# Kernel tuning notes

Hardware: AMD Instinct MI355X
Metric: run time of the kernel (lower is better)

Reference implementation:

```python
import jax, jax.numpy as jnp
import numpy as np

N, D_IN, H, OUT, L = 6144, 512, 512, 256, 3
EPS = 1e-5


def setup_inputs() -> dict:
    key = jax.random.key(0)
    ks = jax.random.split(key, 32)
    inp = {}
    inp["X"] = jax.random.normal(ks[0], (N, D_IN), dtype=jnp.float32)
    inp["adj"] = jax.random.randint(ks[1], (N, N), 0, 2).astype(jnp.float32)
    inp["adj_glo"] = jax.random.randint(ks[2], (N, N), 0, 2).astype(jnp.float32)
    s = 1.0 / np.sqrt(H)
    # projection + its BN
    inp["Wp"] = jax.random.normal(ks[3], (H, D_IN), dtype=jnp.float32) / np.sqrt(D_IN)
    inp["bp"] = jnp.zeros((H,), jnp.float32)
    inp["gp"] = jnp.ones((H,), jnp.float32)
    inp["betap"] = jnp.zeros((H,), jnp.float32)
    # per-layer params; layers 0,1 output H, layer 2 outputs OUT
    outs = [H, H, OUT]
    for i in range(L):
        o = outs[i]
        k = jax.random.split(ks[4 + i], 6)
        inp[f"Wq{i}"] = jax.random.normal(k[0], (H, H), jnp.float32) * s
        inp[f"Wk{i}"] = jax.random.normal(k[1], (H, H), jnp.float32) * s
        inp[f"Wv{i}"] = jax.random.normal(k[2], (H, H), jnp.float32) * s
        inp[f"Wo{i}"] = jax.random.normal(k[3], (o, H), jnp.float32) * s
        inp[f"bo{i}"] = jnp.zeros((o,), jnp.float32)
        inp[f"g{i}"] = jnp.ones((o,), jnp.float32)
        inp[f"beta{i}"] = jnp.zeros((o,), jnp.float32)
    return inp


def _normalize_adj(a):
    # symmetric GCN normalization D^{-1/2} A D^{-1/2}
    d = a.sum(axis=1)
    dis = jnp.where(d > 0, jax.lax.rsqrt(jnp.maximum(d, 1e-12)), 0.0)
    return a * dis[:, None] * dis[None, :]


def _bn(x, g, b):
    # BatchNorm1d, training mode: batch stats, biased variance
    m = x.mean(axis=0)
    v = x.var(axis=0)
    return g * (x - m) * jax.lax.rsqrt(v + EPS) + b


def _attn(h, adj, Wq, Wk, Wv, Wo, bo):
    Q = h @ Wq.T
    K = h @ Wk.T
    V = h @ Wv.T
    scores = (Q @ K.T) / np.sqrt(H)            # [N, N]
    scores = jnp.where(adj == 0, -jnp.inf, scores)
    attn = jax.nn.softmax(scores, axis=-1)
    return (attn @ V) @ Wo.T + bo


def reference(X, adj, adj_glo, Wp, bp, gp, betap,
              Wq0, Wk0, Wv0, Wo0, bo0, g0, beta0,
              Wq1, Wk1, Wv1, Wo1, bo1, g1, beta1,
              Wq2, Wk2, Wv2, Wo2, bo2, g2, beta2):
    # embedding: normalized global adjacency aggregation + projection + BN
    h = _normalize_adj(adj_glo) @ X
    h = h @ Wp.T + bp
    h = _bn(h, gp, betap)
    embed_features = h
    layers = [
        (Wq0, Wk0, Wv0, Wo0, bo0, g0, beta0),
        (Wq1, Wk1, Wv1, Wo1, bo1, g1, beta1),
        (Wq2, Wk2, Wv2, Wo2, bo2, g2, beta2),
    ]
    for i, (Wq, Wk, Wv, Wo, bo, g, b) in enumerate(layers):
        h_s = h
        h = _attn(h, adj, Wq, Wk, Wv, Wo, bo)
        h = jax.nn.relu(_bn(h, g, b))
        if i != L - 1:
            h = h + h_s
    return h, embed_features
```

## Files before the change

kernel.cpp:

```cpp
#include <hip/hip_runtime.h>
#include <cstdint>

#define NROW 6144
#define HDIM 512
#define DOUT 256
#define NEG_INF (-__builtin_inff())

typedef _Float16 half8 __attribute__((ext_vector_type(8)));
typedef _Float16 half4v __attribute__((ext_vector_type(4)));
typedef float f32x4 __attribute__((ext_vector_type(4)));

#define BARRIER() asm volatile("s_barrier" ::: "memory")
#define LGKM0()   asm volatile("s_waitcnt lgkmcnt(0)" ::: "memory")
#define VMCNT4()  asm volatile("s_waitcnt vmcnt(4)" ::: "memory")
#define VMCNT0()  asm volatile("s_waitcnt vmcnt(0)" ::: "memory")

__device__ __forceinline__ void gld_lds16(void* lds, const void* g) {
  __builtin_amdgcn_global_load_lds(
      (const __attribute__((address_space(1))) void*)g,
      (__attribute__((address_space(3))) void*)lds, 16, 0, 0);
}

__global__ __launch_bounds__(512, 2)
void gemm256(const _Float16* __restrict__ A, int lda,
             const _Float16* __restrict__ B, int ldb,
             _Float16* __restrict__ C, int ldc, int Kc, long MN)
{
  __shared__ _Float16 As[2][256][64];
  __shared__ _Float16 Bs[2][256][64];
  const int tid = threadIdx.x;
  const int wave = tid >> 6, lane = tid & 63;
  const int wr = wave >> 2, wc = wave & 3;

  const int gx = gridDim.x, gy = gridDim.y;
  const int nwg = gx * gy * gridDim.z;
  int lin = (blockIdx.z * gy + blockIdx.y) * gx + blockIdx.x;
  int swz = (nwg % 8 == 0) ? ((lin % 8) * (nwg >> 3) + (lin >> 3)) : lin;
  const int bx = swz % gx, by = (swz / gx) % gy, bz = swz / (gx * gy);
  const int row0 = bx * 256, col0 = by * 256;
  const _Float16* Ab = A + (size_t)row0 * lda + (size_t)bz * Kc;
  const _Float16* Bb = B + (size_t)col0 * ldb + (size_t)bz * Kc;
  const int nt = Kc >> 6;

  const int srow = lane >> 3;
  const int sgr  = (lane & 7) ^ srow;

  auto stageA = [&](int buf, int h, int t) {
    const _Float16* src = Ab + (size_t)(h * 128 + wave * 8 + srow) * lda + t * 64 + sgr * 8;
    gld_lds16(&As[buf][h * 128 + wave * 8][0], src);
    gld_lds16(&As[buf][h * 128 + 64 + wave * 8][0], src + (size_t)64 * lda);
  };
  auto stageB = [&](int buf, int h, int t) {
    const _Float16* src = Bb + (size_t)(h * 128 + wave * 8 + srow) * ldb + t * 64 + sgr * 8;
    gld_lds16(&Bs[buf][h * 128 + wave * 8][0], src);
    gld_lds16(&Bs[buf][h * 128 + 64 + wave * 8][0], src + (size_t)64 * ldb);
  };

  const int fr = lane & 15, sq = lane >> 4, fx = fr & 7;
  half8 af[4][2], bLo[2][2], bHi[2][2];
  f32x4 acc[8][4];
  const f32x4 vzero = {0.f, 0.f, 0.f, 0.f};
  #pragma unroll
  for (int f = 0; f < 8; ++f)
    #pragma unroll
    for (int j = 0; j < 4; ++j)
      acc[f][j] = vzero;

  auto dsA = [&](int buf, int mh) {
    #pragma unroll
    for (int i = 0; i < 4; ++i)
      #pragma unroll
      for (int ks = 0; ks < 2; ++ks)
        af[i][ks] = *(const half8*)&As[buf][wr * 128 + mh * 64 + i * 16 + fr]
                                          [((ks * 4 + sq) ^ fx) * 8];
  };
  auto dsBlo = [&](int buf) {
    #pragma unroll
    for (int jj = 0; jj < 2; ++jj)
      #pragma unroll
      for (int ks = 0; ks < 2; ++ks)
        bLo[jj][ks] = *(const half8*)&Bs[buf][wc * 64 + jj * 16 + fr]
                                            [((ks * 4 + sq) ^ fx) * 8];
  };
  auto dsBhi = [&](int buf) {
    #pragma unroll
    for (int jj = 0; jj < 2; ++jj)
      #pragma unroll
      for (int ks = 0; ks < 2; ++ks)
        bHi[jj][ks] = *(const half8*)&Bs[buf][wc * 64 + 32 + jj * 16 + fr]
                                            [((ks * 4 + sq) ^ fx) * 8];
  };
  auto mQlo = [&](int fb) {
    __builtin_amdgcn_s_setprio(1);
    #pragma unroll
    for (int i = 0; i < 4; ++i)
      #pragma unroll
      for (int jj = 0; jj < 2; ++jj)
        #pragma unroll
        for (int ks = 0; ks < 2; ++ks)
          acc[fb + i][jj] = __builtin_amdgcn_mfma_f32_16x16x32_f16(
              af[i][ks], bLo[jj][ks], acc[fb + i][jj], 0, 0, 0);
    __builtin_amdgcn_s_setprio(0);
  };
  auto mQhi = [&](int fb) {
    __builtin_amdgcn_s_setprio(1);
    #pragma unroll
    for (int i = 0; i < 4; ++i)
      #pragma unroll
      for (int jj = 0; jj < 2; ++jj)
        #pragma unroll
        for (int ks = 0; ks < 2; ++ks)
          acc[fb + i][2 + jj] = __builtin_amdgcn_mfma_f32_16x16x32_f16(
              af[i][ks], bHi[jj][ks], acc[fb + i][2 + jj], 0, 0, 0);
    __builtin_amdgcn_s_setprio(0);
  };

  stageA(0, 0, 0); stageA(0, 1, 0); stageB(0, 0, 0); stageB(0, 1, 0);
  stageB(1, 0, 1); stageB(1, 1, 1);
  VMCNT4();
  BARRIER();

  for (int T = 0; T < nt; T += 2) {
    const bool pipe = (T + 2 < nt);
    dsA(0, 0); dsBlo(0);
    stageA(1, 0, T + 1);
    BARRIER(); LGKM0(); mQlo(0); BARRIER();
    dsBhi(0);
    stageA(1, 1, T + 1);
    BARRIER(); LGKM0(); mQhi(0); BARRIER();
    dsA(0, 1);
    if (pipe) stageB(0, 0, T + 2);
    BARRIER(); LGKM0(); mQhi(4); BARRIER();
    if (pipe) { stageB(0, 1, T + 2); VMCNT4(); } else { VMCNT0(); }
    BARRIER(); mQlo(4); BARRIER();
    dsA(1, 0); dsBlo(1);
    if (pipe) stageA(0, 0, T + 2);
    BARRIER(); LGKM0(); mQlo(0); BARRIER();
    dsBhi(1);
    if (pipe) stageA(0, 1, T + 2);
    BARRIER(); LGKM0(); mQhi(0); BARRIER();
    dsA(1, 1);
    if (pipe) stageB(1, 0, T + 3);
    BARRIER(); LGKM0(); mQhi(4); BARRIER();
    if (pipe) { stageB(1, 1, T + 3); VMCNT4(); } else { VMCNT0(); }
    BARRIER(); mQlo(4); BARRIER();
  }

  _Float16* dst = C + (size_t)bz * MN;
  #pragma unroll
  for (int f = 0; f < 8; ++f)
    #pragma unroll
    for (int j = 0; j < 4; ++j)
      #pragma unroll
      for (int r = 0; r < 4; ++r) {
        int row = row0 + wr * 128 + f * 16 + sq * 4 + r;
        int col = col0 + wc * 64 + j * 16 + fr;
        dst[(size_t)row * ldc + col] = (_Float16)acc[f][j][r];
      }
}

__global__ __launch_bounds__(256)
void gemm_f16(const _Float16* __restrict__ A, int lda,
              const _Float16* __restrict__ B, int ldb,
              float* __restrict__ Cf, _Float16* __restrict__ Ch, int ldc,
              int Kc, _Float16* __restrict__ Pk, long MN)
{
  __shared__ _Float16 As[128][32];
  __shared__ _Float16 Bs[128][32];
  const int tid = threadIdx.x;
  const int wave = tid >> 6, lane = tid & 63;
  const int wr = wave >> 1, wc = wave & 1;
  const int row0 = blockIdx.x * 128, col0 = blockIdx.y * 128;
  const int kbase = blockIdx.z * Kc;

  const int sr = lane >> 2;
  const int sk = ((lane & 3) ^ ((lane >> 3) & 3)) * 8;

  f32x4 acc[4][4];
  const f32x4 vzero = {0.f, 0.f, 0.f, 0.f};
  #pragma unroll
  for (int i = 0; i < 4; ++i)
    #pragma unroll
    for (int j = 0; j < 4; ++j)
      acc[i][j] = vzero;

  const int fr = lane & 15;
  const int fk = (((lane >> 4) ^ ((fr >> 1) & 3))) * 8;

  for (int k0 = kbase; k0 < kbase + Kc; k0 += 32) {
    #pragma unroll
    for (int c = 0; c < 2; ++c) {
      int rbase = c * 64 + wave * 16;
      gld_lds16(&As[rbase][0], A + (size_t)(row0 + rbase + sr) * lda + k0 + sk);
      gld_lds16(&Bs[rbase][0], B + (size_t)(col0 + rbase + sr) * ldb + k0 + sk);
    }
    __syncthreads();
    half8 af[4], bf[4];
    #pragma unroll
    for (int i = 0; i < 4; ++i)
      af[i] = *(const half8*)&As[wr * 64 + i * 16 + fr][fk];
    #pragma unroll
    for (int j = 0; j < 4; ++j)
      bf[j] = *(const half8*)&Bs[wc * 64 + j * 16 + fr][fk];
    #pragma unroll
    for (int i = 0; i < 4; ++i)
      #pragma unroll
      for (int j = 0; j < 4; ++j)
        acc[i][j] = __builtin_amdgcn_mfma_f32_16x16x32_f16(af[i], bf[j], acc[i][j], 0, 0, 0);
    __syncthreads();
  }

  const int lr = (lane >> 4) * 4;
  const int lc = lane & 15;
  if (Pk) {
    _Float16* dst = Pk + (size_t)blockIdx.z * MN;
    #pragma unroll
    for (int i = 0; i < 4; ++i)
      #pragma unroll
      for (int j = 0; j < 4; ++j)
        #pragma unroll
        for (int r = 0; r < 4; ++r) {
          int row = row0 + wr * 64 + i * 16 + lr + r;
          int col = col0 + wc * 64 + j * 16 + lc;
          dst[(size_t)row * ldc + col] = (_Float16)acc[i][j][r];
        }
    return;
  }
  #pragma unroll
  for (int i = 0; i < 4; ++i)
    #pragma unroll
    for (int j = 0; j < 4; ++j)
      #pragma unroll
      for (int r = 0; r < 4; ++r) {
        int row = row0 + wr * 64 + i * 16 + lr + r;
        int col = col0 + wc * 64 + j * 16 + lc;
        float v = acc[i][j][r];
        if (Cf) Cf[(size_t)row * ldc + col] = v;
        if (Ch) Ch[(size_t)row * ldc + col] = (_Float16)v;
      }
}

__global__ __launch_bounds__(256)
void reduce_splitk(const _Float16* __restrict__ Pk, long MN, int S, int cshift,
                   const float* __restrict__ rowscale,
                   float* __restrict__ Yf, _Float16* __restrict__ Yh)
{
  long n4 = MN >> 2;
  for (long i = (long)blockIdx.x * 256 + threadIdx.x; i < n4; i += (long)gridDim.x * 256) {
    float s0 = 0, s1 = 0, s2 = 0, s3 = 0;
    for (int z = 0; z < S; ++z) {
      half4v p = ((const half4v*)(Pk + (size_t)z * MN))[i];
      s0 += (float)p[0]; s1 += (float)p[1]; s2 += (float)p[2]; s3 += (float)p[3];
    }
    if (rowscale) {
      float sc = rowscale[(i * 4) >> cshift];
      s0 *= sc; s1 *= sc; s2 *= sc; s3 *= sc;
    }
    if (Yf) {
      float4 o; o.x = s0; o.y = s1; o.z = s2; o.w = s3;
      ((float4*)Yf)[i] = o;
    }
    if (Yh) {
      half4v o;
      o[0] = (_Float16)s0; o[1] = (_Float16)s1; o[2] = (_Float16)s2; o[3] = (_Float16)s3;
      ((half4v*)Yh)[i] = o;
    }
  }
}

__global__ __launch_bounds__(256)
void degree_convert(const float* __restrict__ A, _Float16* __restrict__ Ah,
                    float* __restrict__ dis)
{
  const int row = blockIdx.x;
  const float* a = A + (size_t)row * NROW;
  _Float16* o = Ah + (size_t)row * NROW;
  float s = 0.f;
  #pragma unroll
  for (int it = 0; it < 6; ++it) {
    int j = it * 1024 + threadIdx.x * 4;
    float4 v = *(const float4*)&a[j];
    s += v.x + v.y + v.z + v.w;
    half4v h;
    h[0] = (_Float16)v.x; h[1] = (_Float16)v.y; h[2] = (_Float16)v.z; h[3] = (_Float16)v.w;
    *(half4v*)&o[j] = h;
  }
  #pragma unroll
  for (int off = 32; off; off >>= 1) s += __shfl_xor(s, off);
  __shared__ float red[4];
  if ((threadIdx.x & 63) == 0) red[threadIdx.x >> 6] = s;
  __syncthreads();
  if (threadIdx.x == 0) {
    float d = red[0] + red[1] + red[2] + red[3];
    dis[row] = (d > 0.f) ? rsqrtf(fmaxf(d, 1e-12f)) : 0.f;
  }
}

__global__ __launch_bounds__(192)
void build_mask(const float* __restrict__ adj, uint32_t* __restrict__ bits)
{
  const int row = blockIdx.x;
  const int w = threadIdx.x;
  const float* a = adj + (size_t)row * NROW + w * 32;
  uint32_t m = 0;
  #pragma unroll
  for (int q = 0; q < 8; ++q) {
    float4 x = *(const float4*)&a[q * 4];
    m |= (x.x != 0.f ? 1u : 0u) << (q * 4 + 0);
    m |= (x.y != 0.f ? 1u : 0u) << (q * 4 + 1);
    m |= (x.z != 0.f ? 1u : 0u) << (q * 4 + 2);
    m |= (x.w != 0.f ? 1u : 0u) << (q * 4 + 3);
  }
  bits[(size_t)row * 192 + w] = m;
}

struct WConv {
  const float* src[13];
  _Float16* dst[13];
  int n4[13];
  float scale[13];
};
__global__ __launch_bounds__(256)
void convert_weights(WConv w)
{
  const int seg = blockIdx.x >> 4;
  const int bi = blockIdx.x & 15;
  const float* x = w.src[seg];
  _Float16* y = w.dst[seg];
  const float sc = w.scale[seg];
  const int n4 = w.n4[seg];
  for (int i = bi * 256 + threadIdx.x; i < n4; i += 16 * 256) {
    float4 v = ((const float4*)x)[i];
    half4v o;
    o[0] = (_Float16)(v.x * sc); o[1] = (_Float16)(v.y * sc);
    o[2] = (_Float16)(v.z * sc); o[3] = (_Float16)(v.w * sc);
    ((half4v*)y)[i] = o;
  }
}

__global__ __launch_bounds__(256)
void transpose_scale_f16(const float* __restrict__ src, const float* __restrict__ rowscale,
                         _Float16* __restrict__ dst, int R, int C)
{
  __shared__ _Float16 tile[64][72];
  const int c0 = blockIdx.x * 64, r0 = blockIdx.y * 64;
  const int tx4 = (threadIdx.x & 15) * 4, ty = threadIdx.x >> 4;
  #pragma unroll
  for (int p = 0; p < 4; ++p) {
    int r = p * 16 + ty;
    float4 v = *(const float4*)&src[(size_t)(r0 + r) * C + c0 + tx4];
    float sc = rowscale ? rowscale[r0 + r] : 1.0f;
    tile[tx4 + 0][r] = (_Float16)(v.x * sc);
    tile[tx4 + 1][r] = (_Float16)(v.y * sc);
    tile[tx4 + 2][r] = (_Float16)(v.z * sc);
    tile[tx4 + 3][r] = (_Float16)(v.w * sc);
  }
  __syncthreads();
  #pragma unroll
  for (int p = 0; p < 4; ++p) {
    int c = p * 16 + ty;
    half4v o;
    o[0] = tile[c][tx4 + 0];
    o[1] = tile[c][tx4 + 1];
    o[2] = tile[c][tx4 + 2];
    o[3] = tile[c][tx4 + 3];
    *(half4v*)&dst[(size_t)(c0 + c) * R + r0 + tx4] = o;
  }
}

__global__ __launch_bounds__(256)
void transpose_f16(const _Float16* __restrict__ src, int ld,
                   _Float16* __restrict__ dst, int R, int C)
{
  __shared__ _Float16 tile[64][72];
  const int c0 = blockIdx.x * 64, r0 = blockIdx.y * 64;
  const int tx4 = (threadIdx.x & 15) * 4, ty = threadIdx.x >> 4;
  #pragma unroll
  for (int p = 0; p < 4; ++p) {
    int r = p * 16 + ty;
    half4v v = *(const half4v*)&src[(size_t)(r0 + r) * ld + c0 + tx4];
    tile[tx4 + 0][r] = v[0];
    tile[tx4 + 1][r] = v[1];
    tile[tx4 + 2][r] = v[2];
    tile[tx4 + 3][r] = v[3];
  }
  __syncthreads();
  #pragma unroll
  for (int p = 0; p < 4; ++p) {
    int c = p * 16 + ty;
    half4v o;
    o[0] = tile[c][tx4 + 0];
    o[1] = tile[c][tx4 + 1];
    o[2] = tile[c][tx4 + 2];
    o[3] = tile[c][tx4 + 3];
    *(half4v*)&dst[(size_t)(c0 + c) * R + r0 + tx4] = o;
  }
}

__global__ __launch_bounds__(256)
void softmax_mask16(_Float16* __restrict__ Sf, const uint32_t* __restrict__ bits,
                    float* __restrict__ linv)
{
  const int row = blockIdx.x;
  _Float16* s = Sf + (size_t)row * NROW;
  const uint32_t* b = bits + (size_t)row * 192;
  const int tid = threadIdx.x;
  float v[24];
  float m = NEG_INF;
  #pragma unroll
  for (int it = 0; it < 3; ++it) {
    int j = it * 2048 + tid * 8;
    half8 sv = *(const half8*)&s[j];
    uint32_t w = (b[j >> 5] >> (j & 31)) & 0xffu;
    #pragma unroll
    for (int e = 0; e < 8; ++e) {
      float x = ((w >> e) & 1u) ? (float)sv[e] : NEG_INF;
      v[it * 8 + e] = x;
      m = fmaxf(m, x);
    }
  }
  #pragma unroll
  for (int off = 32; off; off >>= 1) m = fmaxf(m, __shfl_xor(m, off));
  __shared__ float red[4];
  const int lane = tid & 63, wave = tid >> 6;
  if (lane == 0) red[wave] = m;
  __syncthreads();
  m = fmaxf(fmaxf(red[0], red[1]), fmaxf(red[2], red[3]));
  __syncthreads();
  float l = 0.f;
  #pragma unroll
  for (int k = 0; k < 24; ++k) {
    float e = (v[k] == NEG_INF) ? 0.f : __expf(v[k] - m);
    v[k] = e; l += e;
  }
  #pragma unroll
  for (int off = 32; off; off >>= 1) l += __shfl_xor(l, off);
  if (lane == 0) red[wave] = l;
  __syncthreads();
  l = red[0] + red[1] + red[2] + red[3];
  if (tid == 0) linv[row] = (l > 0.f) ? (1.f / l) : 0.f;
  #pragma unroll
  for (int it = 0; it < 3; ++it) {
    int j = it * 2048 + tid * 8;
    half8 o;
    #pragma unroll
    for (int e = 0; e < 8; ++e) o[e] = (_Float16)v[it * 8 + e];
    *(half8*)&s[j] = o;
  }
}

__global__ __launch_bounds__(256)
void bn_partial(const _Float16* __restrict__ X, int C,
                float* __restrict__ psum, float* __restrict__ psq)
{
  const int b = blockIdx.x;
  const int t = threadIdx.x;
  const int tpc = C >> 3;
  const int ng = 256 / tpc;
  const int g = t / tpc, c8 = (t % tpc) * 8;
  const int rpg = 64 / ng;
  const _Float16* x = X + (size_t)b * 64 * C;
  float s[8], q[8];
  #pragma unroll
  for (int e = 0; e < 8; ++e) { s[e] = 0.f; q[e] = 0.f; }
  for (int r = g * rpg; r < (g + 1) * rpg; ++r) {
    half8 v = *(const half8*)&x[(size_t)r * C + c8];
    #pragma unroll
    for (int e = 0; e < 8; ++e) {
      float f = (float)v[e];
      s[e] += f; q[e] += f * f;
    }
  }
  __shared__ float ls[256][8], lq[256][8];
  #pragma unroll
  for (int e = 0; e < 8; ++e) { ls[t][e] = s[e]; lq[t][e] = q[e]; }
  __syncthreads();
  for (int u = t; u < C; u += 256) {
    float ss = 0, qq = 0;
    for (int gg = 0; gg < ng; ++gg) {
      ss += ls[gg * tpc + (u >> 3)][u & 7];
      qq += lq[gg * tpc + (u >> 3)][u & 7];
    }
    psum[b * C + u] = ss; psq[b * C + u] = qq;
  }
}

__global__ void bn_finalize(const float* __restrict__ psum, const float* __restrict__ psq,
                            int C, const float* __restrict__ g, const float* __restrict__ beta,
                            float* __restrict__ scale, float* __restrict__ shift)
{
  int c = threadIdx.x + blockIdx.x * blockDim.x;
  if (c >= C) return;
  float s = 0, q = 0;
  for (int b = 0; b < 96; ++b) { s += psum[b * C + c]; q += psq[b * C + c]; }
  const float invN = 1.0f / 6144.0f;
  float mean = s * invN;
  float var = q * invN - mean * mean;
  float rstd = rsqrtf(fmaxf(var, 0.f) + 1e-5f);
  float sc = g[c] * rstd;
  scale[c] = sc;
  shift[c] = beta[c] - mean * sc;
}

__global__ __launch_bounds__(256)
void bn_apply(const _Float16* __restrict__ X, const float* __restrict__ scale,
              const float* __restrict__ shift, const _Float16* __restrict__ residual,
              float* __restrict__ Yf, _Float16* __restrict__ Yh,
              int Cmask, long total, int do_relu)
{
  for (long i = (long)blockIdx.x * 256 + threadIdx.x; i < total; i += (long)gridDim.x * 256) {
    int c = (int)(i & Cmask);
    float v = (float)X[i] * scale[c] + shift[c];
    if (do_relu) v = fmaxf(v, 0.f);
    if (residual) v += (float)residual[i];
    if (Yf) Yf[i] = v;
    if (Yh) Yh[i] = (_Float16)v;
  }
}

extern "C" void kernel_launch(void* const* d_in, const int* in_sizes, int n_in,
                              void* d_out, int out_size, void* d_ws, size_t ws_size,
                              hipStream_t stream)
{
  (void)in_sizes; (void)n_in; (void)out_size; (void)ws_size;
  const float* X     = (const float*)d_in[0];
  const float* adj   = (const float*)d_in[1];
  const float* adjg  = (const float*)d_in[2];
  const float* Wp    = (const float*)d_in[3];
  const float* gp    = (const float*)d_in[5];
  const float* betap = (const float*)d_in[6];

  float* out_h     = (float*)d_out;
  float* out_embed = out_h + (size_t)NROW * DOUT;

  char* base = (char*)d_ws;
  size_t off = 0;
  auto alloc = [&](size_t bytes) -> void* {
    void* p = base + off;
    off += (bytes + 255) & ~(size_t)255;
    return p;
  };

  const long MN512 = (long)NROW * 512;

  _Float16* Ag  = (_Float16*)alloc((size_t)NROW * NROW * 2);
  _Float16* Sf  = Ag;
  uint32_t* bits = (uint32_t*)alloc((size_t)NROW * 192 * 4);
  _Float16* Pk  = (_Float16*)alloc((size_t)8 * MN512 * 2);
  _Float16* XsT = (_Float16*)alloc((size_t)HDIM * NROW * 2);
  _Float16* Yh16 = (_Float16*)alloc((size_t)NROW * HDIM * 2);
  _Float16* Wph = (_Float16*)alloc((size_t)HDIM * HDIM * 2);
  _Float16* QKVW[3];
  for (int i = 0; i < 3; ++i) QKVW[i] = (_Float16*)alloc((size_t)1536 * HDIM * 2);
  _Float16* Woh[3];
  Woh[0] = (_Float16*)alloc((size_t)512 * 512 * 2);
  Woh[1] = (_Float16*)alloc((size_t)512 * 512 * 2);
  Woh[2] = (_Float16*)alloc((size_t)256 * 512 * 2);
  _Float16* QKVh = (_Float16*)alloc((size_t)NROW * 1536 * 2);
  _Float16* VTh  = (_Float16*)alloc((size_t)HDIM * NROW * 2);
  _Float16* AVh  = (_Float16*)alloc((size_t)NROW * HDIM * 2);
  _Float16* xh   = (_Float16*)alloc((size_t)NROW * HDIM * 2);
  _Float16* hb16A = (_Float16*)alloc((size_t)NROW * HDIM * 2);
  _Float16* hb16B = (_Float16*)alloc((size_t)NROW * HDIM * 2);
  float* dis  = (float*)alloc((size_t)NROW * 4);
  float* linv = (float*)alloc((size_t)NROW * 4);
  float* psum = (float*)alloc((size_t)96 * 512 * 4);
  float* psq  = (float*)alloc((size_t)96 * 512 * 4);
  float* bnsc = (float*)alloc(512 * 4);
  float* bnsh = (float*)alloc(512 * 4);

  const float qk_scale = 0.21022410381342863f;

  degree_convert<<<NROW, 256, 0, stream>>>(adjg, Ag, dis);
  build_mask<<<NROW, 192, 0, stream>>>(adj, bits);
  transpose_scale_f16<<<dim3(8, 96), 256, 0, stream>>>(X, dis, XsT, NROW, HDIM);

  {
    WConv w;
    int seg = 0;
    w.src[seg] = Wp; w.dst[seg] = Wph; w.n4[seg] = 512 * 512 / 4; w.scale[seg] = 1.f; ++seg;
    for (int i = 0; i < 3; ++i) {
      int o = (i < 2) ? 512 : 256;
      w.src[seg] = (const float*)d_in[7 + i * 7 + 0]; w.dst[seg] = QKVW[i];
      w.n4[seg] = 512 * 512 / 4; w.scale[seg] = qk_scale; ++seg;
      w.src[seg] = (const float*)d_in[7 + i * 7 + 1]; w.dst[seg] = QKVW[i] + 512 * 512;
      w.n4[seg] = 512 * 512 / 4; w.scale[seg] = qk_scale; ++seg;
      w.src[seg] = (const float*)d_in[7 + i * 7 + 2]; w.dst[seg] = QKVW[i] + 2 * 512 * 512;
      w.n4[seg] = 512 * 512 / 4; w.scale[seg] = 1.f; ++seg;
      w.src[seg] = (const float*)d_in[7 + i * 7 + 3]; w.dst[seg] = Woh[i];
      w.n4[seg] = o * 512 / 4; w.scale[seg] = 1.f; ++seg;
    }
    convert_weights<<<13 * 16, 256, 0, stream>>>(w);
  }

  gemm256<<<dim3(24, 2, 8), 512, 0, stream>>>(Ag, NROW, XsT, NROW, Pk, 512, 768, MN512);
  reduce_splitk<<<1536, 256, 0, stream>>>(Pk, MN512, 8, 9, dis, nullptr, Yh16);
  gemm_f16<<<dim3(48, 4), 256, 0, stream>>>(Yh16, HDIM, Wph, HDIM, nullptr, xh, HDIM,
                                            512, nullptr, 0);
  bn_partial<<<96, 256, 0, stream>>>(xh, 512, psum, psq);
  bn_finalize<<<2, 256, 0, stream>>>(psum, psq, 512, gp, betap, bnsc, bnsh);
  bn_apply<<<2048, 256, 0, stream>>>(xh, bnsc, bnsh, nullptr, out_embed, hb16A,
                                     511, MN512, 0);

  _Float16* hbuf[2] = {hb16A, hb16B};
  int cur = 0;
  for (int i = 0; i < 3; ++i) {
    int o = (i < 2) ? 512 : 256;
    const float* gl = (const float*)d_in[7 + i * 7 + 5];
    const float* bl = (const float*)d_in[7 + i * 7 + 6];
    _Float16* hin = hbuf[cur];

    gemm_f16<<<dim3(48, 12), 256, 0, stream>>>(hin, HDIM, QKVW[i], HDIM, nullptr, QKVh, 1536,
                                               512, nullptr, 0);
    transpose_f16<<<dim3(8, 96), 256, 0, stream>>>(QKVh + 1024, 1536, VTh, NROW, HDIM);
    gemm256<<<dim3(24, 24), 512, 0, stream>>>(QKVh, 1536, QKVh + 512, 1536, Sf, NROW, 512, 0);
    softmax_mask16<<<NROW, 256, 0, stream>>>(Sf, bits, linv);
    gemm256<<<dim3(24, 2, 8), 512, 0, stream>>>(Sf, NROW, VTh, NROW, Pk, 512, 768, MN512);
    reduce_splitk<<<1536, 256, 0, stream>>>(Pk, MN512, 8, 9, linv, nullptr, AVh);
    long MNo = (long)NROW * o;
    gemm_f16<<<dim3(48, o / 128, 4), 256, 0, stream>>>(AVh, HDIM, Woh[i], HDIM,
                                                       nullptr, nullptr, o, 128, Pk, MNo);
    reduce_splitk<<<1536, 256, 0, stream>>>(Pk, MNo, 4, (o == 512) ? 9 : 8, nullptr,
                                            nullptr, xh);
    bn_partial<<<96, 256, 0, stream>>>(xh, o, psum, psq);
    bn_finalize<<<2, 256, 0, stream>>>(psum, psq, o, gl, bl, bnsc, bnsh);
    if (i < 2) {
      bn_apply<<<2048, 256, 0, stream>>>(xh, bnsc, bnsh, hin, nullptr, hbuf[cur ^ 1],
                                         o - 1, (long)NROW * o, 1);
      cur ^= 1;
    } else {
      bn_apply<<<2048, 256, 0, stream>>>(xh, bnsc, bnsh, nullptr, out_h, nullptr,
                                         o - 1, (long)NROW * o, 1);
    }
  }
}
```

Baseline: 834.7 us.

## Fuse masked softmax statistics into QK GEMM epilogue and exp into PV GEMM

```diff
diff --git a/kernel.cpp b/kernel.cpp
--- a/kernel.cpp
+++ b/kernel.cpp
@@ -4,7 +4,7 @@
 #define NROW 6144
 #define HDIM 512
 #define DOUT 256
-#define NEG_INF (-__builtin_inff())
+#define FNEG (-3.0e38f)
 
 typedef _Float16 half8 __attribute__((ext_vector_type(8)));
 typedef _Float16 half4v __attribute__((ext_vector_type(4)));
@@ -24,10 +24,14 @@
 __global__ __launch_bounds__(512, 2)
 void gemm256(const _Float16* __restrict__ A, int lda,
              const _Float16* __restrict__ B, int ldb,
-             _Float16* __restrict__ C, int ldc, int Kc, long MN)
+             _Float16* __restrict__ C, int ldc, int Kc, long MN,
+             const uint32_t* __restrict__ bits,
+             float* __restrict__ Mp, float* __restrict__ Lp)
 {
   __shared__ _Float16 As[2][256][64];
   __shared__ _Float16 Bs[2][256][64];
+  __shared__ float Msh[256][4];
+  __shared__ float Lsh[256][4];
   const int tid = threadIdx.x;
   const int wave = tid >> 6, lane = tid & 63;
   const int wr = wave >> 2, wc = wave & 3;
@@ -157,6 +161,231 @@
         int col = col0 + wc * 64 + j * 16 + fr;
         dst[(size_t)row * ldc + col] = (_Float16)acc[f][j][r];
       }
+
+  if (Mp) {
+    #pragma unroll
+    for (int f = 0; f < 8; ++f)
+      #pragma unroll
+      for (int r = 0; r < 4; ++r) {
+        int rl = wr * 128 + f * 16 + sq * 4 + r;
+        size_t bbase = (size_t)(row0 + rl) * 192 + (col0 >> 5) + wc * 2;
+        uint32_t b0 = bits[bbase], b1 = bits[bbase + 1];
+        float s0 = (float)(_Float16)acc[f][0][r];
+        float s1 = (float)(_Float16)acc[f][1][r];
+        float s2 = (float)(_Float16)acc[f][2][r];
+        float s3 = (float)(_Float16)acc[f][3][r];
+        uint32_t k0 = (b0 >> fr) & 1u, k1 = (b0 >> (16 + fr)) & 1u;
+        uint32_t k2 = (b1 >> fr) & 1u, k3 = (b1 >> (16 + fr)) & 1u;
+        float mx = fmaxf(fmaxf(k0 ? s0 : FNEG, k1 ? s1 : FNEG),
+                         fmaxf(k2 ? s2 : FNEG, k3 ? s3 : FNEG));
+        #pragma unroll
+        for (int off = 1; off < 16; off <<= 1) mx = fmaxf(mx, __shfl_xor(mx, off));
+        float l = (k0 ? __expf(s0 - mx) : 0.f) + (k1 ? __expf(s1 - mx) : 0.f) +
+                  (k2 ? __expf(s2 - mx) : 0.f) + (k3 ? __expf(s3 - mx) : 0.f);
+        #pragma unroll
+        for (int off = 1; off < 16; off <<= 1) l += __shfl_xor(l, off);
+        if (fr == 0) { Msh[rl][wc] = mx; Lsh[rl][wc] = l; }
+      }
+    __syncthreads();
+    if (tid < 256) {
+      float m0 = Msh[tid][0], m1 = Msh[tid][1], m2 = Msh[tid][2], m3 = Msh[tid][3];
+      float mx = fmaxf(fmaxf(m0, m1), fmaxf(m2, m3));
+      float l = Lsh[tid][0] * __expf(m0 - mx) + Lsh[tid][1] * __expf(m1 - mx) +
+                Lsh[tid][2] * __expf(m2 - mx) + Lsh[tid][3] * __expf(m3 - mx);
+      Mp[(size_t)by * NROW + row0 + tid] = mx;
+      Lp[(size_t)by * NROW + row0 + tid] = l;
+    }
+  }
+}
+
+__global__ __launch_bounds__(512, 2)
+void gemm256_pv(const _Float16* __restrict__ S,
+                const _Float16* __restrict__ B, int ldb,
+                const uint32_t* __restrict__ bits,
+                const float* __restrict__ mrow,
+                _Float16* __restrict__ Pk, int Kc, long MN)
+{
+  __shared__ _Float16 As[2][256][64];
+  __shared__ _Float16 Bs[2][256][64];
+  const int tid = threadIdx.x;
+  const int wave = tid >> 6, lane = tid & 63;
+  const int wr = wave >> 2, wc = wave & 3;
+
+  const int gx = gridDim.x, gy = gridDim.y;
+  const int nwg = gx * gy * gridDim.z;
+  int lin = (blockIdx.z * gy + blockIdx.y) * gx + blockIdx.x;
+  int swz = (nwg % 8 == 0) ? ((lin % 8) * (nwg >> 3) + (lin >> 3)) : lin;
+  const int bx = swz % gx, by = (swz / gx) % gy, bz = swz / (gx * gy);
+  const int row0 = bx * 256, col0 = by * 256;
+  const _Float16* Bb = B + (size_t)col0 * ldb + (size_t)bz * Kc;
+  const int kbase = bz * Kc;
+  const int nt = Kc >> 6;
+
+  const int srow = lane >> 3;
+  const int sg   = lane & 7;
+  const int sgr  = sg ^ srow;
+
+  auto stageB = [&](int buf, int h, int t) {
+    const _Float16* src = Bb + (size_t)(h * 128 + wave * 8 + srow) * ldb + t * 64 + sgr * 8;
+    gld_lds16(&Bs[buf][h * 128 + wave * 8][0], src);
+    gld_lds16(&Bs[buf][h * 128 + 64 + wave * 8][0], src + (size_t)64 * ldb);
+  };
+
+  float mv[2][2];
+  #pragma unroll
+  for (int h = 0; h < 2; ++h)
+    #pragma unroll
+    for (int p = 0; p < 2; ++p)
+      mv[h][p] = mrow[row0 + h * 128 + p * 64 + wave * 8 + srow];
+
+  half8 rA[2][2][2];
+  uint32_t rM[2][2][2];
+  auto ISSUE = [&](int buf, int h, int t) {
+    int kb = kbase + t * 64;
+    const _Float16* s0 = S + (size_t)(row0 + h * 128 + wave * 8 + srow) * NROW + kb + sg * 8;
+    rA[buf][h][0] = *(const half8*)s0;
+    rA[buf][h][1] = *(const half8*)(s0 + (size_t)64 * NROW);
+    const uint32_t* bw = bits + (size_t)(row0 + h * 128 + wave * 8 + srow) * 192
+                              + (kb >> 5) + (sg >> 2);
+    rM[buf][h][0] = *bw;
+    rM[buf][h][1] = *(bw + (size_t)64 * 192);
+  };
+  auto WRITE = [&](int buf, int h) {
+    #pragma unroll
+    for (int p = 0; p < 2; ++p) {
+      int row = h * 128 + p * 64 + wave * 8 + srow;
+      float m = mv[h][p];
+      uint32_t w = (rM[buf][h][p] >> ((sg & 3) * 8)) & 0xffu;
+      half8 sv = rA[buf][h][p];
+      half8 e;
+      #pragma unroll
+      for (int k = 0; k < 8; ++k)
+        e[k] = (_Float16)(((w >> k) & 1u) ? __expf((float)sv[k] - m) : 0.f);
+      *(half8*)&As[buf][row][(sg ^ srow) * 8] = e;
+    }
+  };
+
+  const int fr = lane & 15, sq = lane >> 4, fx = fr & 7;
+  half8 af[4][2], bLo[2][2], bHi[2][2];
+  f32x4 acc[8][4];
+  const f32x4 vzero = {0.f, 0.f, 0.f, 0.f};
+  #pragma unroll
+  for (int f = 0; f < 8; ++f)
+    #pragma unroll
+    for (int j = 0; j < 4; ++j)
+      acc[f][j] = vzero;
+
+  auto dsA = [&](int buf, int mh) {
+    #pragma unroll
+    for (int i = 0; i < 4; ++i)
+      #pragma unroll
+      for (int ks = 0; ks < 2; ++ks)
+        af[i][ks] = *(const half8*)&As[buf][wr * 128 + mh * 64 + i * 16 + fr]
+                                          [((ks * 4 + sq) ^ fx) * 8];
+  };
+  auto dsBlo = [&](int buf) {
+    #pragma unroll
+    for (int jj = 0; jj < 2; ++jj)
+      #pragma unroll
+      for (int ks = 0; ks < 2; ++ks)
+        bLo[jj][ks] = *(const half8*)&Bs[buf][wc * 64 + jj * 16 + fr]
+                                            [((ks * 4 + sq) ^ fx) * 8];
+  };
+  auto dsBhi = [&](int buf) {
+    #pragma unroll
+    for (int jj = 0; jj < 2; ++jj)
+      #pragma unroll
+      for (int ks = 0; ks < 2; ++ks)
+        bHi[jj][ks] = *(const half8*)&Bs[buf][wc * 64 + 32 + jj * 16 + fr]
+                                            [((ks * 4 + sq) ^ fx) * 8];
+  };
+  auto mQlo = [&](int fb) {
+    __builtin_amdgcn_s_setprio(1);
+    #pragma unroll
+    for (int i = 0; i < 4; ++i)
+      #pragma unroll
+      for (int jj = 0; jj < 2; ++jj)
+        #pragma unroll
+        for (int ks = 0; ks < 2; ++ks)
+          acc[fb + i][jj] = __builtin_amdgcn_mfma_f32_16x16x32_f16(
+              af[i][ks], bLo[jj][ks], acc[fb + i][jj], 0, 0, 0);
+    __builtin_amdgcn_s_setprio(0);
+  };
+  auto mQhi = [&](int fb) {
+    __builtin_amdgcn_s_setprio(1);
+    #pragma unroll
+    for (int i = 0; i < 4; ++i)
+      #pragma unroll
+      for (int jj = 0; jj < 2; ++jj)
+        #pragma unroll
+        for (int ks = 0; ks < 2; ++ks)
+          acc[fb + i][2 + jj] = __builtin_amdgcn_mfma_f32_16x16x32_f16(
+              af[i][ks], bHi[jj][ks], acc[fb + i][2 + jj], 0, 0, 0);
+    __builtin_amdgcn_s_setprio(0);
+  };
+
+  ISSUE(0, 0, 0); ISSUE(0, 1, 0); ISSUE(1, 0, 1); ISSUE(1, 1, 1);
+  stageB(0, 0, 0); stageB(0, 1, 0); stageB(1, 0, 1); stageB(1, 1, 1);
+  VMCNT4();
+  WRITE(0, 0); WRITE(0, 1);
+  LGKM0();
+  BARRIER();
+
+  for (int T = 0; T < nt; T += 2) {
+    const bool pipe = (T + 2 < nt);
+    dsA(0, 0); dsBlo(0);
+    WRITE(1, 0);
+    if (pipe) ISSUE(0, 0, T + 2);
+    BARRIER(); LGKM0(); mQlo(0); BARRIER();
+    dsBhi(0);
+    WRITE(1, 1);
+    if (pipe) ISSUE(0, 1, T + 2);
+    BARRIER(); LGKM0(); mQhi(0); BARRIER();
+    dsA(0, 1);
+    if (pipe) stageB(0, 0, T + 2);
+    BARRIER(); LGKM0(); mQhi(4); BARRIER();
+    if (pipe) { stageB(0, 1, T + 2); VMCNT4(); } else { VMCNT0(); }
+    BARRIER(); mQlo(4); BARRIER();
+    dsA(1, 0); dsBlo(1);
+    if (pipe) { WRITE(0, 0); ISSUE(1, 0, T + 3); }
+    BARRIER(); LGKM0(); mQlo(0); BARRIER();
+    dsBhi(1);
+    if (pipe) { WRITE(0, 1); ISSUE(1, 1, T + 3); }
+    BARRIER(); LGKM0(); mQhi(0); BARRIER();
+    dsA(1, 1);
+    if (pipe) stageB(1, 0, T + 3);
+    BARRIER(); LGKM0(); mQhi(4); BARRIER();
+    if (pipe) { stageB(1, 1, T + 3); VMCNT4(); } else { VMCNT0(); }
+    BARRIER(); mQlo(4); BARRIER();
+  }
+
+  _Float16* dst = Pk + (size_t)bz * MN;
+  #pragma unroll
+  for (int f = 0; f < 8; ++f)
+    #pragma unroll
+    for (int j = 0; j < 4; ++j)
+      #pragma unroll
+      for (int r = 0; r < 4; ++r) {
+        int row = row0 + wr * 128 + f * 16 + sq * 4 + r;
+        int col = col0 + wc * 64 + j * 16 + fr;
+        dst[(size_t)row * 512 + col] = (_Float16)acc[f][j][r];
+      }
+}
+
+__global__ __launch_bounds__(256)
+void stats_reduce(const float* __restrict__ Mp, const float* __restrict__ Lp,
+                  float* __restrict__ mrow, float* __restrict__ linv)
+{
+  int row = blockIdx.x * 256 + threadIdx.x;
+  float mx = FNEG;
+  #pragma unroll 4
+  for (int b = 0; b < 24; ++b) mx = fmaxf(mx, Mp[(size_t)b * NROW + row]);
+  float l = 0.f;
+  #pragma unroll 4
+  for (int b = 0; b < 24; ++b)
+    l += Lp[(size_t)b * NROW + row] * __expf(Mp[(size_t)b * NROW + row] - mx);
+  mrow[row] = mx;
+  linv[row] = (l > 0.f) ? (1.f / l) : 0.f;
 }
 
 __global__ __launch_bounds__(256)
@@ -269,49 +498,50 @@
 }
 
 __global__ __launch_bounds__(256)
-void degree_convert(const float* __restrict__ A, _Float16* __restrict__ Ah,
-                    float* __restrict__ dis)
-{
-  const int row = blockIdx.x;
-  const float* a = A + (size_t)row * NROW;
-  _Float16* o = Ah + (size_t)row * NROW;
-  float s = 0.f;
-  #pragma unroll
-  for (int it = 0; it < 6; ++it) {
-    int j = it * 1024 + threadIdx.x * 4;
-    float4 v = *(const float4*)&a[j];
-    s += v.x + v.y + v.z + v.w;
-    half4v h;
-    h[0] = (_Float16)v.x; h[1] = (_Float16)v.y; h[2] = (_Float16)v.z; h[3] = (_Float16)v.w;
-    *(half4v*)&o[j] = h;
-  }
-  #pragma unroll
-  for (int off = 32; off; off >>= 1) s += __shfl_xor(s, off);
-  __shared__ float red[4];
-  if ((threadIdx.x & 63) == 0) red[threadIdx.x >> 6] = s;
-  __syncthreads();
-  if (threadIdx.x == 0) {
-    float d = red[0] + red[1] + red[2] + red[3];
-    dis[row] = (d > 0.f) ? rsqrtf(fmaxf(d, 1e-12f)) : 0.f;
-  }
-}
-
-__global__ __launch_bounds__(192)
-void build_mask(const float* __restrict__ adj, uint32_t* __restrict__ bits)
-{
-  const int row = blockIdx.x;
-  const int w = threadIdx.x;
-  const float* a = adj + (size_t)row * NROW + w * 32;
-  uint32_t m = 0;
-  #pragma unroll
-  for (int q = 0; q < 8; ++q) {
-    float4 x = *(const float4*)&a[q * 4];
-    m |= (x.x != 0.f ? 1u : 0u) << (q * 4 + 0);
-    m |= (x.y != 0.f ? 1u : 0u) << (q * 4 + 1);
-    m |= (x.z != 0.f ? 1u : 0u) << (q * 4 + 2);
-    m |= (x.w != 0.f ? 1u : 0u) << (q * 4 + 3);
-  }
-  bits[(size_t)row * 192 + w] = m;
+void prep_adj(const float* __restrict__ Aglo, _Float16* __restrict__ Ah,
+              float* __restrict__ dis, const float* __restrict__ adj,
+              uint32_t* __restrict__ bits)
+{
+  if (blockIdx.x < NROW) {
+    const int row = blockIdx.x;
+    const float* a = Aglo + (size_t)row * NROW;
+    _Float16* o = Ah + (size_t)row * NROW;
+    float s = 0.f;
+    #pragma unroll
+    for (int it = 0; it < 6; ++it) {
+      int j = it * 1024 + threadIdx.x * 4;
+      float4 v = *(const float4*)&a[j];
+      s += v.x + v.y + v.z + v.w;
+      half4v h;
+      h[0] = (_Float16)v.x; h[1] = (_Float16)v.y; h[2] = (_Float16)v.z; h[3] = (_Float16)v.w;
+      *(half4v*)&o[j] = h;
+    }
+    #pragma unroll
+    for (int off = 32; off; off >>= 1) s += __shfl_xor(s, off);
+    __shared__ float red[4];
+    if ((threadIdx.x & 63) == 0) red[threadIdx.x >> 6] = s;
+    __syncthreads();
+    if (threadIdx.x == 0) {
+      float d = red[0] + red[1] + red[2] + red[3];
+      dis[row] = (d > 0.f) ? rsqrtf(fmaxf(d, 1e-12f)) : 0.f;
+    }
+  } else {
+    const int row = blockIdx.x - NROW;
+    const int w = threadIdx.x;
+    if (w < 192) {
+      const float* a = adj + (size_t)row * NROW + w * 32;
+      uint32_t m = 0;
+      #pragma unroll
+      for (int q = 0; q < 8; ++q) {
+        float4 x = *(const float4*)&a[q * 4];
+        m |= (x.x != 0.f ? 1u : 0u) << (q * 4 + 0);
+        m |= (x.y != 0.f ? 1u : 0u) << (q * 4 + 1);
+        m |= (x.z != 0.f ? 1u : 0u) << (q * 4 + 2);
+        m |= (x.w != 0.f ? 1u : 0u) << (q * 4 + 3);
+      }
+      bits[(size_t)row * 192 + w] = m;
+    }
+  }
 }
 
 struct WConv {
@@ -398,58 +628,6 @@
 }
 
 __global__ __launch_bounds__(256)
-void softmax_mask16(_Float16* __restrict__ Sf, const uint32_t* __restrict__ bits,
-                    float* __restrict__ linv)
-{
-  const int row = blockIdx.x;
-  _Float16* s = Sf + (size_t)row * NROW;
-  const uint32_t* b = bits + (size_t)row * 192;
-  const int tid = threadIdx.x;
-  float v[24];
-  float m = NEG_INF;
-  #pragma unroll
-  for (int it = 0; it < 3; ++it) {
-    int j = it * 2048 + tid * 8;
-    half8 sv = *(const half8*)&s[j];
-    uint32_t w = (b[j >> 5] >> (j & 31)) & 0xffu;
-    #pragma unroll
-    for (int e = 0; e < 8; ++e) {
-      float x = ((w >> e) & 1u) ? (float)sv[e] : NEG_INF;
-      v[it * 8 + e] = x;
-      m = fmaxf(m, x);
-    }
-  }
-  #pragma unroll
-  for (int off = 32; off; off >>= 1) m = fmaxf(m, __shfl_xor(m, off));
-  __shared__ float red[4];
-  const int lane = tid & 63, wave = tid >> 6;
-  if (lane == 0) red[wave] = m;
-  __syncthreads();
-  m = fmaxf(fmaxf(red[0], red[1]), fmaxf(red[2], red[3]));
-  __syncthreads();
-  float l = 0.f;
-  #pragma unroll
-  for (int k = 0; k < 24; ++k) {
-    float e = (v[k] == NEG_INF) ? 0.f : __expf(v[k] - m);
-    v[k] = e; l += e;
-  }
-  #pragma unroll
-  for (int off = 32; off; off >>= 1) l += __shfl_xor(l, off);
-  if (lane == 0) red[wave] = l;
-  __syncthreads();
-  l = red[0] + red[1] + red[2] + red[3];
-  if (tid == 0) linv[row] = (l > 0.f) ? (1.f / l) : 0.f;
-  #pragma unroll
-  for (int it = 0; it < 3; ++it) {
-    int j = it * 2048 + tid * 8;
-    half8 o;
-    #pragma unroll
-    for (int e = 0; e < 8; ++e) o[e] = (_Float16)v[it * 8 + e];
-    *(half8*)&s[j] = o;
-  }
-}
-
-__global__ __launch_bounds__(256)
 void bn_partial(const _Float16* __restrict__ X, int C,
                 float* __restrict__ psum, float* __restrict__ psq)
 {
@@ -546,7 +724,7 @@
   _Float16* Ag  = (_Float16*)alloc((size_t)NROW * NROW * 2);
   _Float16* Sf  = Ag;
   uint32_t* bits = (uint32_t*)alloc((size_t)NROW * 192 * 4);
-  _Float16* Pk  = (_Float16*)alloc((size_t)8 * MN512 * 2);
+  _Float16* Pk  = (_Float16*)alloc((size_t)6 * MN512 * 2);
   _Float16* XsT = (_Float16*)alloc((size_t)HDIM * NROW * 2);
   _Float16* Yh16 = (_Float16*)alloc((size_t)NROW * HDIM * 2);
   _Float16* Wph = (_Float16*)alloc((size_t)HDIM * HDIM * 2);
@@ -563,7 +741,10 @@
   _Float16* hb16A = (_Float16*)alloc((size_t)NROW * HDIM * 2);
   _Float16* hb16B = (_Float16*)alloc((size_t)NROW * HDIM * 2);
   float* dis  = (float*)alloc((size_t)NROW * 4);
+  float* mrow = (float*)alloc((size_t)NROW * 4);
   float* linv = (float*)alloc((size_t)NROW * 4);
+  float* Mpart = (float*)alloc((size_t)24 * NROW * 4);
+  float* Lpart = (float*)alloc((size_t)24 * NROW * 4);
   float* psum = (float*)alloc((size_t)96 * 512 * 4);
   float* psq  = (float*)alloc((size_t)96 * 512 * 4);
   float* bnsc = (float*)alloc(512 * 4);
@@ -571,8 +752,7 @@
 
   const float qk_scale = 0.21022410381342863f;
 
-  degree_convert<<<NROW, 256, 0, stream>>>(adjg, Ag, dis);
-  build_mask<<<NROW, 192, 0, stream>>>(adj, bits);
+  prep_adj<<<2 * NROW, 256, 0, stream>>>(adjg, Ag, dis, adj, bits);
   transpose_scale_f16<<<dim3(8, 96), 256, 0, stream>>>(X, dis, XsT, NROW, HDIM);
 
   {
@@ -593,8 +773,9 @@
     convert_weights<<<13 * 16, 256, 0, stream>>>(w);
   }
 
-  gemm256<<<dim3(24, 2, 8), 512, 0, stream>>>(Ag, NROW, XsT, NROW, Pk, 512, 768, MN512);
-  reduce_splitk<<<1536, 256, 0, stream>>>(Pk, MN512, 8, 9, dis, nullptr, Yh16);
+  gemm256<<<dim3(24, 2, 6), 512, 0, stream>>>(Ag, NROW, XsT, NROW, Pk, 512, 1024, MN512,
+                                              nullptr, nullptr, nullptr);
+  reduce_splitk<<<1536, 256, 0, stream>>>(Pk, MN512, 6, 9, dis, nullptr, Yh16);
   gemm_f16<<<dim3(48, 4), 256, 0, stream>>>(Yh16, HDIM, Wph, HDIM, nullptr, xh, HDIM,
                                             512, nullptr, 0);
   bn_partial<<<96, 256, 0, stream>>>(xh, 512, psum, psq);
@@ -613,10 +794,11 @@
     gemm_f16<<<dim3(48, 12), 256, 0, stream>>>(hin, HDIM, QKVW[i], HDIM, nullptr, QKVh, 1536,
                                                512, nullptr, 0);
     transpose_f16<<<dim3(8, 96), 256, 0, stream>>>(QKVh + 1024, 1536, VTh, NROW, HDIM);
-    gemm256<<<dim3(24, 24), 512, 0, stream>>>(QKVh, 1536, QKVh + 512, 1536, Sf, NROW, 512, 0);
-    softmax_mask16<<<NROW, 256, 0, stream>>>(Sf, bits, linv);
-    gemm256<<<dim3(24, 2, 8), 512, 0, stream>>>(Sf, NROW, VTh, NROW, Pk, 512, 768, MN512);
-    reduce_splitk<<<1536, 256, 0, stream>>>(Pk, MN512, 8, 9, linv, nullptr, AVh);
+    gemm256<<<dim3(24, 24), 512, 0, stream>>>(QKVh, 1536, QKVh + 512, 1536, Sf, NROW, 512, 0,
+                                              bits, Mpart, Lpart);
+    stats_reduce<<<24, 256, 0, stream>>>(Mpart, Lpart, mrow, linv);
+    gemm256_pv<<<dim3(24, 2, 6), 512, 0, stream>>>(Sf, VTh, NROW, bits, mrow, Pk, 1024, MN512);
+    reduce_splitk<<<1536, 256, 0, stream>>>(Pk, MN512, 6, 9, linv, nullptr, AVh);
     long MNo = (long)NROW * o;
     gemm_f16<<<dim3(48, o / 128, 4), 256, 0, stream>>>(AVh, HDIM, Woh[i], HDIM,
                                                        nullptr, nullptr, o, 128, Pk, MNo);
```

Result: slower. 1.287 ms (+54.1%).

## Fuse BN partial stats into split-K reduce, merge adj prep, compute V transposed

Applied to the files above, without the earlier changes.

```diff
diff --git a/kernel.cpp b/kernel.cpp
--- a/kernel.cpp
+++ b/kernel.cpp
@@ -243,9 +243,11 @@
 __global__ __launch_bounds__(256)
 void reduce_splitk(const _Float16* __restrict__ Pk, long MN, int S, int cshift,
                    const float* __restrict__ rowscale,
-                   float* __restrict__ Yf, _Float16* __restrict__ Yh)
+                   float* __restrict__ Yf, _Float16* __restrict__ Yh,
+                   float* __restrict__ psum, float* __restrict__ psq, int C)
 {
   long n4 = MN >> 2;
+  float bs[4] = {0.f, 0.f, 0.f, 0.f}, bq[4] = {0.f, 0.f, 0.f, 0.f};
   for (long i = (long)blockIdx.x * 256 + threadIdx.x; i < n4; i += (long)gridDim.x * 256) {
     float s0 = 0, s1 = 0, s2 = 0, s3 = 0;
     for (int z = 0; z < S; ++z) {
@@ -264,54 +266,84 @@
       half4v o;
       o[0] = (_Float16)s0; o[1] = (_Float16)s1; o[2] = (_Float16)s2; o[3] = (_Float16)s3;
       ((half4v*)Yh)[i] = o;
-    }
-  }
-}
-
-__global__ __launch_bounds__(256)
-void degree_convert(const float* __restrict__ A, _Float16* __restrict__ Ah,
-                    float* __restrict__ dis)
-{
-  const int row = blockIdx.x;
-  const float* a = A + (size_t)row * NROW;
-  _Float16* o = Ah + (size_t)row * NROW;
-  float s = 0.f;
-  #pragma unroll
-  for (int it = 0; it < 6; ++it) {
-    int j = it * 1024 + threadIdx.x * 4;
-    float4 v = *(const float4*)&a[j];
-    s += v.x + v.y + v.z + v.w;
-    half4v h;
-    h[0] = (_Float16)v.x; h[1] = (_Float16)v.y; h[2] = (_Float16)v.z; h[3] = (_Float16)v.w;
-    *(half4v*)&o[j] = h;
-  }
-  #pragma unroll
-  for (int off = 32; off; off >>= 1) s += __shfl_xor(s, off);
-  __shared__ float red[4];
-  if ((threadIdx.x & 63) == 0) red[threadIdx.x >> 6] = s;
-  __syncthreads();
-  if (threadIdx.x == 0) {
-    float d = red[0] + red[1] + red[2] + red[3];
-    dis[row] = (d > 0.f) ? rsqrtf(fmaxf(d, 1e-12f)) : 0.f;
-  }
-}
-
-__global__ __launch_bounds__(192)
-void build_mask(const float* __restrict__ adj, uint32_t* __restrict__ bits)
-{
-  const int row = blockIdx.x;
-  const int w = threadIdx.x;
-  const float* a = adj + (size_t)row * NROW + w * 32;
-  uint32_t m = 0;
-  #pragma unroll
-  for (int q = 0; q < 8; ++q) {
-    float4 x = *(const float4*)&a[q * 4];
-    m |= (x.x != 0.f ? 1u : 0u) << (q * 4 + 0);
-    m |= (x.y != 0.f ? 1u : 0u) << (q * 4 + 1);
-    m |= (x.z != 0.f ? 1u : 0u) << (q * 4 + 2);
-    m |= (x.w != 0.f ? 1u : 0u) << (q * 4 + 3);
-  }
-  bits[(size_t)row * 192 + w] = m;
+      if (psum) {
+        #pragma unroll
+        for (int e = 0; e < 4; ++e) {
+          float v = (float)o[e];
+          bs[e] += v; bq[e] += v * v;
+        }
+      }
+    }
+  }
+  if (psum) {
+    __shared__ float ls[256][4], lq[256][4];
+    const int t = threadIdx.x;
+    #pragma unroll
+    for (int e = 0; e < 4; ++e) { ls[t][e] = bs[e]; lq[t][e] = bq[e]; }
+    __syncthreads();
+    const int cg = C >> 2;
+    if (t < cg) {
+      float ss[4] = {0, 0, 0, 0}, qq[4] = {0, 0, 0, 0};
+      for (int g = 0; g < 256 / cg; ++g)
+        #pragma unroll
+        for (int e = 0; e < 4; ++e) {
+          ss[e] += ls[t + g * cg][e];
+          qq[e] += lq[t + g * cg][e];
+        }
+      #pragma unroll
+      for (int e = 0; e < 4; ++e) {
+        psum[(size_t)blockIdx.x * C + t * 4 + e] = ss[e];
+        psq[(size_t)blockIdx.x * C + t * 4 + e] = qq[e];
+      }
+    }
+  }
+}
+
+__global__ __launch_bounds__(256)
+void prep_adj(const float* __restrict__ Aglo, _Float16* __restrict__ Ah,
+              float* __restrict__ dis, const float* __restrict__ adj,
+              uint32_t* __restrict__ bits)
+{
+  if (blockIdx.x < NROW) {
+    const int row = blockIdx.x;
+    const float* a = Aglo + (size_t)row * NROW;
+    _Float16* o = Ah + (size_t)row * NROW;
+    float s = 0.f;
+    #pragma unroll
+    for (int it = 0; it < 6; ++it) {
+      int j = it * 1024 + threadIdx.x * 4;
+      float4 v = *(const float4*)&a[j];
+      s += v.x + v.y + v.z + v.w;
+      half4v h;
+      h[0] = (_Float16)v.x; h[1] = (_Float16)v.y; h[2] = (_Float16)v.z; h[3] = (_Float16)v.w;
+      *(half4v*)&o[j] = h;
+    }
+    #pragma unroll
+    for (int off = 32; off; off >>= 1) s += __shfl_xor(s, off);
+    __shared__ float red[4];
+    if ((threadIdx.x & 63) == 0) red[threadIdx.x >> 6] = s;
+    __syncthreads();
+    if (threadIdx.x == 0) {
+      float d = red[0] + red[1] + red[2] + red[3];
+      dis[row] = (d > 0.f) ? rsqrtf(fmaxf(d, 1e-12f)) : 0.f;
+    }
+  } else {
+    const int row = blockIdx.x - NROW;
+    const int w = threadIdx.x;
+    if (w < 192) {
+      const float* a = adj + (size_t)row * NROW + w * 32;
+      uint32_t m = 0;
+      #pragma unroll
+      for (int q = 0; q < 8; ++q) {
+        float4 x = *(const float4*)&a[q * 4];
+        m |= (x.x != 0.f ? 1u : 0u) << (q * 4 + 0);
+        m |= (x.y != 0.f ? 1u : 0u) << (q * 4 + 1);
+        m |= (x.z != 0.f ? 1u : 0u) << (q * 4 + 2);
+        m |= (x.w != 0.f ? 1u : 0u) << (q * 4 + 3);
+      }
+      bits[(size_t)row * 192 + w] = m;
+    }
+  }
 }
 
 struct WConv {
@@ -369,35 +401,6 @@
 }
 
 __global__ __launch_bounds__(256)
-void transpose_f16(const _Float16* __restrict__ src, int ld,
-                   _Float16* __restrict__ dst, int R, int C)
-{
-  __shared__ _Float16 tile[64][72];
-  const int c0 = blockIdx.x * 64, r0 = blockIdx.y * 64;
-  const int tx4 = (threadIdx.x & 15) * 4, ty = threadIdx.x >> 4;
-  #pragma unroll
-  for (int p = 0; p < 4; ++p) {
-    int r = p * 16 + ty;
-    half4v v = *(const half4v*)&src[(size_t)(r0 + r) * ld + c0 + tx4];
-    tile[tx4 + 0][r] = v[0];
-    tile[tx4 + 1][r] = v[1];
-    tile[tx4 + 2][r] = v[2];
-    tile[tx4 + 3][r] = v[3];
-  }
-  __syncthreads();
-  #pragma unroll
-  for (int p = 0; p < 4; ++p) {
-    int c = p * 16 + ty;
-    half4v o;
-    o[0] = tile[c][tx4 + 0];
-    o[1] = tile[c][tx4 + 1];
-    o[2] = tile[c][tx4 + 2];
-    o[3] = tile[c][tx4 + 3];
-    *(half4v*)&dst[(size_t)(c0 + c) * R + r0 + tx4] = o;
-  }
-}
-
-__global__ __launch_bounds__(256)
 void softmax_mask16(_Float16* __restrict__ Sf, const uint32_t* __restrict__ bits,
                     float* __restrict__ linv)
 {
@@ -486,13 +489,14 @@
 }
 
 __global__ void bn_finalize(const float* __restrict__ psum, const float* __restrict__ psq,
-                            int C, const float* __restrict__ g, const float* __restrict__ beta,
+                            int C, int nb,
+                            const float* __restrict__ g, const float* __restrict__ beta,
                             float* __restrict__ scale, float* __restrict__ shift)
 {
   int c = threadIdx.x + blockIdx.x * blockDim.x;
   if (c >= C) return;
   float s = 0, q = 0;
-  for (int b = 0; b < 96; ++b) { s += psum[b * C + c]; q += psq[b * C + c]; }
+  for (int b = 0; b < nb; ++b) { s += psum[(size_t)b * C + c]; q += psq[(size_t)b * C + c]; }
   const float invN = 1.0f / 6144.0f;
   float mean = s * invN;
   float var = q * invN - mean * mean;
@@ -556,7 +560,7 @@
   Woh[0] = (_Float16*)alloc((size_t)512 * 512 * 2);
   Woh[1] = (_Float16*)alloc((size_t)512 * 512 * 2);
   Woh[2] = (_Float16*)alloc((size_t)256 * 512 * 2);
-  _Float16* QKVh = (_Float16*)alloc((size_t)NROW * 1536 * 2);
+  _Float16* QKh  = (_Float16*)alloc((size_t)NROW * 1024 * 2);
   _Float16* VTh  = (_Float16*)alloc((size_t)HDIM * NROW * 2);
   _Float16* AVh  = (_Float16*)alloc((size_t)NROW * HDIM * 2);
   _Float16* xh   = (_Float16*)alloc((size_t)NROW * HDIM * 2);
@@ -564,15 +568,14 @@
   _Float16* hb16B = (_Float16*)alloc((size_t)NROW * HDIM * 2);
   float* dis  = (float*)alloc((size_t)NROW * 4);
   float* linv = (float*)alloc((size_t)NROW * 4);
-  float* psum = (float*)alloc((size_t)96 * 512 * 4);
-  float* psq  = (float*)alloc((size_t)96 * 512 * 4);
+  float* psum = (float*)alloc((size_t)1536 * 512 * 4);
+  float* psq  = (float*)alloc((size_t)1536 * 512 * 4);
   float* bnsc = (float*)alloc(512 * 4);
   float* bnsh = (float*)alloc(512 * 4);
 
   const float qk_scale = 0.21022410381342863f;
 
-  degree_convert<<<NROW, 256, 0, stream>>>(adjg, Ag, dis);
-  build_mask<<<NROW, 192, 0, stream>>>(adj, bits);
+  prep_adj<<<2 * NROW, 256, 0, stream>>>(adjg, Ag, dis, adj, bits);
   transpose_scale_f16<<<dim3(8, 96), 256, 0, stream>>>(X, dis, XsT, NROW, HDIM);
 
   {
@@ -594,11 +597,12 @@
   }
 
   gemm256<<<dim3(24, 2, 8), 512, 0, stream>>>(Ag, NROW, XsT, NROW, Pk, 512, 768, MN512);
-  reduce_splitk<<<1536, 256, 0, stream>>>(Pk, MN512, 8, 9, dis, nullptr, Yh16);
+  reduce_splitk<<<1536, 256, 0, stream>>>(Pk, MN512, 8, 9, dis, nullptr, Yh16,
+                                          nullptr, nullptr, 0);
   gemm_f16<<<dim3(48, 4), 256, 0, stream>>>(Yh16, HDIM, Wph, HDIM, nullptr, xh, HDIM,
                                             512, nullptr, 0);
   bn_partial<<<96, 256, 0, stream>>>(xh, 512, psum, psq);
-  bn_finalize<<<2, 256, 0, stream>>>(psum, psq, 512, gp, betap, bnsc, bnsh);
+  bn_finalize<<<2, 256, 0, stream>>>(psum, psq, 512, 96, gp, betap, bnsc, bnsh);
   bn_apply<<<2048, 256, 0, stream>>>(xh, bnsc, bnsh, nullptr, out_embed, hb16A,
                                      511, MN512, 0);
 
@@ -610,20 +614,21 @@
     const float* bl = (const float*)d_in[7 + i * 7 + 6];
     _Float16* hin = hbuf[cur];
 
-    gemm_f16<<<dim3(48, 12), 256, 0, stream>>>(hin, HDIM, QKVW[i], HDIM, nullptr, QKVh, 1536,
-                                               512, nullptr, 0);
-    transpose_f16<<<dim3(8, 96), 256, 0, stream>>>(QKVh + 1024, 1536, VTh, NROW, HDIM);
-    gemm256<<<dim3(24, 24), 512, 0, stream>>>(QKVh, 1536, QKVh + 512, 1536, Sf, NROW, 512, 0);
+    gemm_f16<<<dim3(48, 8), 256, 0, stream>>>(hin, HDIM, QKVW[i], HDIM, nullptr, QKh, 1024,
+                                              512, nullptr, 0);
+    gemm_f16<<<dim3(4, 48), 256, 0, stream>>>(QKVW[i] + 2 * 512 * 512, HDIM, hin, HDIM,
+                                              nullptr, VTh, NROW, 512, nullptr, 0);
+    gemm256<<<dim3(24, 24), 512, 0, stream>>>(QKh, 1024, QKh + 512, 1024, Sf, NROW, 512, 0);
     softmax_mask16<<<NROW, 256, 0, stream>>>(Sf, bits, linv);
     gemm256<<<dim3(24, 2, 8), 512, 0, stream>>>(Sf, NROW, VTh, NROW, Pk, 512, 768, MN512);
-    reduce_splitk<<<1536, 256, 0, stream>>>(Pk, MN512, 8, 9, linv, nullptr, AVh);
+    reduce_splitk<<<1536, 256, 0, stream>>>(Pk, MN512, 8, 9, linv, nullptr, AVh,
+                                            nullptr, nullptr, 0);
     long MNo = (long)NROW * o;
     gemm_f16<<<dim3(48, o / 128, 4), 256, 0, stream>>>(AVh, HDIM, Woh[i], HDIM,
                                                        nullptr, nullptr, o, 128, Pk, MNo);
-    reduce_splitk<<<1536, 256, 0, stream>>>(Pk, MNo, 4, (o == 512) ? 9 : 8, nullptr,
-                                            nullptr, xh);
-    bn_partial<<<96, 256, 0, stream>>>(xh, o, psum, psq);
-    bn_finalize<<<2, 256, 0, stream>>>(psum, psq, o, gl, bl, bnsc, bnsh);
+    reduce_splitk<<<1536, 256, 0, stream>>>(Pk, MNo, 4, 0, nullptr, nullptr, xh,
+                                            psum, psq, o);
+    bn_finalize<<<2, 256, 0, stream>>>(psum, psq, o, 1536, gl, bl, bnsc, bnsh);
     if (i < 2) {
       bn_apply<<<2048, 256, 0, stream>>>(xh, bnsc, bnsh, hin, nullptr, hbuf[cur ^ 1],
                                          o - 1, (long)NROW * o, 1);
```

After: 2.078 ms. 149% more time.
